# Kernel tuning notes

Hardware: AMD Instinct MI355X
Metric: run time of the kernel (lower is better)

The kernel has to match this reference:

```python
import jax, jax.numpy as jnp
import numpy as np

GRID_SIZE = 4
ORDER = 3
NUM_BASIS = GRID_SIZE + ORDER  # 7
KNOTS = jnp.linspace(-1.0, 1.0, NUM_BASIS + ORDER + 1)  # 11 knots


def _normalise(x):
    # eval-mode with uninitialized running stats: use batch min/max
    min_val = x.min(axis=0)
    max_val = x.max(axis=0)
    width = jnp.maximum(max_val - min_val, 0.01)
    centre = 0.5 * (max_val + min_val)
    scaled = (x - centre) / (0.5 * width)
    return jnp.clip(scaled, -2.0, 2.0)


def _bspline_basis(x):
    # x: (B, I) -> basis: (B, I, NUM_BASIS), de Boor recursion vectorized over i
    xe = x[..., None]  # (B, I, 1)
    idx = jnp.arange(NUM_BASIS)
    left, right = KNOTS[idx], KNOTS[idx + 1]
    basis = ((xe >= left) & (xe < right)).astype(x.dtype)
    last = jnp.where(xe[..., 0] == KNOTS[NUM_BASIS], 1.0, basis[..., -1])
    basis = basis.at[..., -1].set(last)
    for k in range(1, ORDER + 1):
        d1 = KNOTS[idx + k] - KNOTS[idx]
        d2 = KNOTS[idx + k + 1] - KNOTS[idx + 1]
        b_next = jnp.concatenate([basis[..., 1:], jnp.zeros_like(basis[..., :1])], axis=-1)
        t1 = jnp.where(d1 > 0, (xe - KNOTS[idx]) / jnp.where(d1 > 0, d1, 1.0), 0.0) * basis
        t2 = jnp.where(d2 > 0, (KNOTS[idx + k + 1] - xe) / jnp.where(d2 > 0, d2, 1.0), 0.0) * b_next
        basis = t1 + t2
    return basis


def setup_inputs() -> dict:
    key = jax.random.key(0)
    k1, k2, k3 = jax.random.split(key, 3)
    B, I, O = 8192, 256, 256
    x = jax.random.normal(k1, (B, I), dtype=jnp.float32)
    # xavier-uniform base_weight
    bound = float(np.sqrt(6.0 / (I + O)))
    base_weight = jax.random.uniform(k2, (O, I), minval=-bound, maxval=bound, dtype=jnp.float32)
    spline_weight = jnp.ones((O, I), dtype=jnp.float32)
    spline_coeff = 0.001 * jax.random.normal(k3, (O, I, NUM_BASIS), dtype=jnp.float32)
    bias = jnp.zeros((O,), dtype=jnp.float32)
    return {"x": x, "base_weight": base_weight, "spline_weight": spline_weight,
            "spline_coeff": spline_coeff, "bias": bias}


def reference(x, base_weight, spline_weight, spline_coeff, bias):
    x_norm = _normalise(x)                          # (B, I)
    basis = _bspline_basis(x_norm)                  # (B, I, M)
    silu_x = x_norm * jax.nn.sigmoid(x_norm)        # (B, I)
    base_out = silu_x @ base_weight.T               # sum_i silu_i * W_oi -> (B, O)
    coeff_scaled = spline_coeff * spline_weight[..., None]  # (O, I, M)
    spline_out = jnp.einsum('bim,oim->bo', basis, coeff_scaled)
    return base_out + spline_out + bias[None, :]
```

## Files before the change

### kernel.cpp

```cpp
#include <hip/hip_runtime.h>
#include <hip/hip_bf16.h>

#define B_SZ 8192
#define I_SZ 256
#define O_SZ 256
#define KDIM 2048
#define BM 32
#define BN 128
#define BKT 64
#define NT 32
#define NPART 128

typedef __bf16 bf16x8 __attribute__((ext_vector_type(8)));
typedef float f32x4 __attribute__((ext_vector_type(4)));

__global__ __launch_bounds__(256) void minmax_partial(
    const float* __restrict__ x, float* __restrict__ pmin,
    float* __restrict__ pmax) {
  const int cg = threadIdx.x & 63;
  const int rs = threadIdx.x >> 6;
  const int r0 = blockIdx.x * 64;
  const float* p = x + (size_t)(r0 + rs) * I_SZ + cg * 4;
  float4 mn = {1e30f, 1e30f, 1e30f, 1e30f};
  float4 mx = {-1e30f, -1e30f, -1e30f, -1e30f};
#pragma unroll
  for (int k = 0; k < 16; ++k) {
    const float4 v = *reinterpret_cast<const float4*>(p + (size_t)k * 4 * I_SZ);
    mn.x = fminf(mn.x, v.x); mn.y = fminf(mn.y, v.y);
    mn.z = fminf(mn.z, v.z); mn.w = fminf(mn.w, v.w);
    mx.x = fmaxf(mx.x, v.x); mx.y = fmaxf(mx.y, v.y);
    mx.z = fmaxf(mx.z, v.z); mx.w = fmaxf(mx.w, v.w);
  }
  __shared__ float rmn[4][I_SZ], rmx[4][I_SZ];
  *reinterpret_cast<float4*>(&rmn[rs][cg * 4]) = mn;
  *reinterpret_cast<float4*>(&rmx[rs][cg * 4]) = mx;
  __syncthreads();
  if (threadIdx.x < 64) {
    float4 a, b;
    const int c0 = threadIdx.x * 4;
    a.x = fminf(fminf(rmn[0][c0+0], rmn[1][c0+0]), fminf(rmn[2][c0+0], rmn[3][c0+0]));
    a.y = fminf(fminf(rmn[0][c0+1], rmn[1][c0+1]), fminf(rmn[2][c0+1], rmn[3][c0+1]));
    a.z = fminf(fminf(rmn[0][c0+2], rmn[1][c0+2]), fminf(rmn[2][c0+2], rmn[3][c0+2]));
    a.w = fminf(fminf(rmn[0][c0+3], rmn[1][c0+3]), fminf(rmn[2][c0+3], rmn[3][c0+3]));
    b.x = fmaxf(fmaxf(rmx[0][c0+0], rmx[1][c0+0]), fmaxf(rmx[2][c0+0], rmx[3][c0+0]));
    b.y = fmaxf(fmaxf(rmx[0][c0+1], rmx[1][c0+1]), fmaxf(rmx[2][c0+1], rmx[3][c0+1]));
    b.z = fmaxf(fmaxf(rmx[0][c0+2], rmx[1][c0+2]), fmaxf(rmx[2][c0+2], rmx[3][c0+2]));
    b.w = fmaxf(fmaxf(rmx[0][c0+3], rmx[1][c0+3]), fmaxf(rmx[2][c0+3], rmx[3][c0+3]));
    *reinterpret_cast<float4*>(&pmin[blockIdx.x * I_SZ + c0]) = a;
    *reinterpret_cast<float4*>(&pmax[blockIdx.x * I_SZ + c0]) = b;
  }
}

__global__ void pack_W(const float* __restrict__ bw,
                       const float* __restrict__ sw,
                       const float* __restrict__ coeff,
                       __hip_bfloat16* __restrict__ W,
                       const float* __restrict__ pmin,
                       const float* __restrict__ pmax,
                       float* __restrict__ cenrhw) {
  const int idx = blockIdx.x * blockDim.x + threadIdx.x;
  const int i = idx & (I_SZ - 1);
  const int o = idx >> 8;
  const float s = sw[idx];
  union { __hip_bfloat16 h[8]; float4 f4; } u;
#pragma unroll
  for (int m = 0; m < 7; ++m)
    u.h[m] = __float2bfloat16(coeff[(size_t)idx * 7 + m] * s);
  u.h[7] = __float2bfloat16(bw[idx]);
  const size_t off = (size_t)o * KDIM + (size_t)((i ^ (o & 7)) << 3);
  *reinterpret_cast<float4*>(&W[off]) = u.f4;

  if (blockIdx.x == 0) {
    const int c = threadIdx.x;
    float mn = 1e30f, mx = -1e30f;
#pragma unroll 8
    for (int p = 0; p < NPART; ++p) {
      mn = fminf(mn, pmin[p * I_SZ + c]);
      mx = fmaxf(mx, pmax[p * I_SZ + c]);
    }
    const float width = fmaxf(mx - mn, 0.01f);
    const float rhw = 2.0f / width;
    cenrhw[2 * c]     = rhw;
    cenrhw[2 * c + 1] = -0.5f * (mx + mn) * rhw;
  }
}

__device__ __forceinline__ void async16(const __hip_bfloat16* g, __hip_bfloat16* l) {
  __builtin_amdgcn_global_load_lds(
      (const __attribute__((address_space(1))) void*)g,
      (__attribute__((address_space(3))) void*)l, 16, 0, 0);
}

__global__ __launch_bounds__(256, 2) void gemm_fused(
    const float* __restrict__ x, const __hip_bfloat16* __restrict__ W,
    const float* __restrict__ cenrhw, const float* __restrict__ bias,
    float* __restrict__ out) {
  __shared__ __align__(16) __hip_bfloat16 Alds[2][BM * BKT];
  __shared__ __align__(16) __hip_bfloat16 Blds[2][BN * BKT];
  __shared__ float2 scl[I_SZ];

  const int t = threadIdx.x;
  const int lane = t & 63;
  const int wave = t >> 6;
  const int fr = lane & 15, fk = lane >> 4;

  const int bid = blockIdx.x;
  const int swz = (bid & 7) * 64 + (bid >> 3);
  const int bm = swz >> 1, bn = swz & 1;
  const int r0 = bm * BM;
  const int c0 = bn * BN;

  scl[t] = reinterpret_cast<const float2*>(cenrhw)[t];

  const int arow = t >> 3;
  const int af_  = t & 7;
  const float* xp = x + (size_t)(r0 + arow) * I_SZ + af_;

  const __hip_bfloat16* gb0 = W + (size_t)(c0 + (t >> 3)) * KDIM + (t & 7) * 8;

  f32x4 acc[2][2] = {{{0.f,0.f,0.f,0.f},{0.f,0.f,0.f,0.f}},
                     {{0.f,0.f,0.f,0.f},{0.f,0.f,0.f,0.f}}};

  auto stageB = [&](int buf, int kt) {
    const size_t k0 = (size_t)kt * BKT;
    async16(gb0 + k0,                      &Blds[buf][t * 8]);
    async16(gb0 + k0 + (size_t)32 * KDIM,  &Blds[buf][2048 + t * 8]);
    async16(gb0 + k0 + (size_t)64 * KDIM,  &Blds[buf][4096 + t * 8]);
    async16(gb0 + k0 + (size_t)96 * KDIM,  &Blds[buf][6144 + t * 8]);
  };

  auto buildA = [&](int buf, int kt, float xv) {
    const float2 s2 = scl[kt * 8 + af_];
    const float xn = __builtin_fmaf(xv, s2.x, s2.y);
    const float sp = __builtin_fmaf(xn, 5.0f, 5.0f);
    const float cf = floorf(sp);
    const float c6 = fminf(cf, 6.0f);
    const int ci = (int)c6;
    const float u = sp - c6;
    const float zm = (sp > 7.0f) ? 0.0f : (1.0f / 6.0f);
    const float u2 = u * u;
    const float u3 = u2 * u;
    const float t1 = 1.0f - u;
    const float q3 = u3 * zm;
    const float q0 = (t1 * t1) * (t1 * zm);
    float h2 = __builtin_fmaf(-3.0f, u, 3.0f);
    h2 = __builtin_fmaf(h2, u, 3.0f);
    h2 = __builtin_fmaf(h2, u, 1.0f);
    const float q2 = h2 * zm;
    float h1 = __builtin_fmaf(3.0f, u, -6.0f);
    h1 = __builtin_fmaf(h1, u2, 4.0f);
    const float q1 = h1 * zm;
    const float silu = xn * __builtin_amdgcn_rcpf(1.0f + __expf(-xn));
    union { __hip_bfloat16 h[8]; float4 f4; } uu;
#pragma unroll
    for (int j = 0; j < 7; ++j) {
      float v = 0.0f;
      v = (ci == j + 3) ? q0 : v;
      v = (ci == j + 2) ? q1 : v;
      v = (ci == j + 1) ? q2 : v;
      v = (ci == j)     ? q3 : v;
      uu.h[j] = __float2bfloat16(v);
    }
    uu.h[7] = __float2bfloat16(silu);
    const int unit = af_ ^ (arow & 7);
    *reinterpret_cast<float4*>(&Alds[buf][arow * BKT + unit * 8]) = uu.f4;
  };

  auto compute = [&](int buf) {
    bf16x8 af[2][2], bg[2][2];
#pragma unroll
    for (int m = 0; m < 2; ++m)
#pragma unroll
      for (int kk = 0; kk < 2; ++kk) {
        const int row = m * 16 + fr;
        const int unit = ((kk << 2) | fk) ^ (row & 7);
        af[m][kk] = *reinterpret_cast<const bf16x8*>(&Alds[buf][row * BKT + unit * 8]);
      }
#pragma unroll
    for (int n = 0; n < 2; ++n)
#pragma unroll
      for (int kk = 0; kk < 2; ++kk) {
        const int row = wave * 32 + n * 16 + fr;
        const int unit = ((kk << 2) | fk) ^ (row & 7);
        bg[n][kk] = *reinterpret_cast<const bf16x8*>(&Blds[buf][row * BKT + unit * 8]);
      }
#pragma unroll
    for (int kk = 0; kk < 2; ++kk)
#pragma unroll
      for (int m = 0; m < 2; ++m)
#pragma unroll
        for (int n = 0; n < 2; ++n)
          acc[m][n] = __builtin_amdgcn_mfma_f32_16x16x32_bf16(
              af[m][kk], bg[n][kk], acc[m][n], 0, 0, 0);
  };

  const float xv0 = xp[0];
  float xpf = xp[8];
  __syncthreads();
  stageB(0, 0);
  buildA(0, 0, xv0);
  __syncthreads();
  int cur = 0;
  for (int kt = 0; kt < NT - 1; ++kt) {
    stageB(cur ^ 1, kt + 1);
    const float xpf2 = xp[min(kt + 2, NT - 1) * 8];
    buildA(cur ^ 1, kt + 1, xpf);
    compute(cur);
    __syncthreads();
    xpf = xpf2;
    cur ^= 1;
  }
  compute(cur);

#pragma unroll
  for (int m = 0; m < 2; ++m)
#pragma unroll
    for (int n = 0; n < 2; ++n) {
      const int col = c0 + wave * 32 + n * 16 + fr;
      const float bc = bias[col];
#pragma unroll
      for (int r = 0; r < 4; ++r) {
        const int row = r0 + m * 16 + fk * 4 + r;
        out[(size_t)row * O_SZ + col] = acc[m][n][r] + bc;
      }
    }
}

extern "C" void kernel_launch(void* const* d_in, const int* in_sizes, int n_in,
                              void* d_out, int out_size, void* d_ws, size_t ws_size,
                              hipStream_t stream) {
  const float* x     = (const float*)d_in[0];
  const float* bw    = (const float*)d_in[1];
  const float* sw    = (const float*)d_in[2];
  const float* coeff = (const float*)d_in[3];
  const float* bias  = (const float*)d_in[4];
  float* out = (float*)d_out;

  char* ws = (char*)d_ws;
  __hip_bfloat16* Wbuf = (__hip_bfloat16*)ws;
  float* pmin   = (float*)(ws + (size_t)O_SZ * KDIM * 2);
  float* pmax   = pmin + NPART * I_SZ;
  float* cenrhw = pmax + NPART * I_SZ;

  minmax_partial<<<NPART, 256, 0, stream>>>(x, pmin, pmax);
  pack_W<<<(O_SZ * I_SZ) / 256, 256, 0, stream>>>(bw, sw, coeff, Wbuf,
                                                  pmin, pmax, cenrhw);
  gemm_fused<<<(B_SZ / BM) * (O_SZ / BN), 256, 0, stream>>>(x, Wbuf, cenrhw,
                                                            bias, out);
}
```

Before: 42.31 us.

## Build spline/SiLU A operand in registers and widen K tile to 128

```diff
diff --git a/kernel.cpp b/kernel.cpp
--- a/kernel.cpp
+++ b/kernel.cpp
@@ -7,8 +7,8 @@
 #define KDIM 2048
 #define BM 32
 #define BN 128
-#define BKT 64
-#define NT 32
+#define KTO 128
+#define NTO 16
 #define NPART 128
 
 typedef __bf16 bf16x8 __attribute__((ext_vector_type(8)));
@@ -95,8 +95,7 @@
     const float* __restrict__ x, const __hip_bfloat16* __restrict__ W,
     const float* __restrict__ cenrhw, const float* __restrict__ bias,
     float* __restrict__ out) {
-  __shared__ __align__(16) __hip_bfloat16 Alds[2][BM * BKT];
-  __shared__ __align__(16) __hip_bfloat16 Blds[2][BN * BKT];
+  __shared__ __align__(16) __hip_bfloat16 Blds[2][BN * KTO];
   __shared__ float2 scl[I_SZ];
 
   const int t = threadIdx.x;
@@ -112,29 +111,26 @@
 
   scl[t] = reinterpret_cast<const float2*>(cenrhw)[t];
 
-  const int arow = t >> 3;
-  const int af_  = t & 7;
-  const float* xp = x + (size_t)(r0 + arow) * I_SZ + af_;
-
-  const __hip_bfloat16* gb0 = W + (size_t)(c0 + (t >> 3)) * KDIM + (t & 7) * 8;
+  const __hip_bfloat16* gbase =
+      W + (size_t)(c0 + (t >> 4)) * KDIM + (t & 15) * 8;
+
+  auto stageB = [&](int buf, int kt) {
+    const __hip_bfloat16* g = gbase + kt * KTO;
+    __hip_bfloat16* l = &Blds[buf][t * 8];
+#pragma unroll
+    for (int q = 0; q < 8; ++q)
+      async16(g + (size_t)16 * q * KDIM, l + 2048 * q);
+  };
+
+  const float* xq = x + (size_t)(r0 + fr) * I_SZ + fk;
 
   f32x4 acc[2][2] = {{{0.f,0.f,0.f,0.f},{0.f,0.f,0.f,0.f}},
                      {{0.f,0.f,0.f,0.f},{0.f,0.f,0.f,0.f}}};
 
-  auto stageB = [&](int buf, int kt) {
-    const size_t k0 = (size_t)kt * BKT;
-    async16(gb0 + k0,                      &Blds[buf][t * 8]);
-    async16(gb0 + k0 + (size_t)32 * KDIM,  &Blds[buf][2048 + t * 8]);
-    async16(gb0 + k0 + (size_t)64 * KDIM,  &Blds[buf][4096 + t * 8]);
-    async16(gb0 + k0 + (size_t)96 * KDIM,  &Blds[buf][6144 + t * 8]);
-  };
-
-  auto buildA = [&](int buf, int kt, float xv) {
-    const float2 s2 = scl[kt * 8 + af_];
+  auto evalOne = [&](float xv, float2 s2) -> bf16x8 {
     const float xn = __builtin_fmaf(xv, s2.x, s2.y);
     const float sp = __builtin_fmaf(xn, 5.0f, 5.0f);
-    const float cf = floorf(sp);
-    const float c6 = fminf(cf, 6.0f);
+    const float c6 = fminf(floorf(sp), 6.0f);
     const int ci = (int)c6;
     const float u = sp - c6;
     const float zm = (sp > 7.0f) ? 0.0f : (1.0f / 6.0f);
@@ -151,7 +147,7 @@
     h1 = __builtin_fmaf(h1, u2, 4.0f);
     const float q1 = h1 * zm;
     const float silu = xn * __builtin_amdgcn_rcpf(1.0f + __expf(-xn));
-    union { __hip_bfloat16 h[8]; float4 f4; } uu;
+    union { __hip_bfloat16 h[8]; bf16x8 v; } uu;
 #pragma unroll
     for (int j = 0; j < 7; ++j) {
       float v = 0.0f;
@@ -162,55 +158,57 @@
       uu.h[j] = __float2bfloat16(v);
     }
     uu.h[7] = __float2bfloat16(silu);
-    const int unit = af_ ^ (arow & 7);
-    *reinterpret_cast<float4*>(&Alds[buf][arow * BKT + unit * 8]) = uu.f4;
+    return uu.v;
   };
 
-  auto compute = [&](int buf) {
-    bf16x8 af[2][2], bg[2][2];
-#pragma unroll
-    for (int m = 0; m < 2; ++m)
-#pragma unroll
-      for (int kk = 0; kk < 2; ++kk) {
-        const int row = m * 16 + fr;
-        const int unit = ((kk << 2) | fk) ^ (row & 7);
-        af[m][kk] = *reinterpret_cast<const bf16x8*>(&Alds[buf][row * BKT + unit * 8]);
+  auto computeTile = [&](int buf, int kt, const float (&xv)[8]) {
+    const __hip_bfloat16* L = Blds[buf];
+    const int brow = wave * 32 + fr;
+    const int bswz = brow & 7;
+#pragma unroll
+    for (int ss = 0; ss < 4; ++ss) {
+      const float2 s2 = scl[kt * 16 + ss * 4 + fk];
+      const bf16x8 a0 = evalOne(xv[ss], s2);
+      const bf16x8 a1 = evalOne(xv[4 + ss], s2);
+      const int u = ((ss << 2) | fk) ^ bswz;
+      const bf16x8 b0 =
+          *reinterpret_cast<const bf16x8*>(&L[brow * KTO + u * 8]);
+      const bf16x8 b1 =
+          *reinterpret_cast<const bf16x8*>(&L[(brow + 16) * KTO + u * 8]);
+      acc[0][0] = __builtin_amdgcn_mfma_f32_16x16x32_bf16(a0, b0, acc[0][0], 0, 0, 0);
+      acc[0][1] = __builtin_amdgcn_mfma_f32_16x16x32_bf16(a0, b1, acc[0][1], 0, 0, 0);
+      acc[1][0] = __builtin_amdgcn_mfma_f32_16x16x32_bf16(a1, b0, acc[1][0], 0, 0, 0);
+      acc[1][1] = __builtin_amdgcn_mfma_f32_16x16x32_bf16(a1, b1, acc[1][1], 0, 0, 0);
+    }
+  };
+
+  float xva[8], xvb[8];
+#pragma unroll
+  for (int j = 0; j < 4; ++j) {
+    xva[j]     = xq[j * 4];
+    xva[4 + j] = xq[16 * I_SZ + j * 4];
+  }
+  stageB(0, 0);
+  __syncthreads();
+
+  for (int kt = 0; kt < NTO; ++kt) {
+    const int buf = kt & 1;
+    if (kt + 1 < NTO) {
+      stageB(buf ^ 1, kt + 1);
+      const int o = (kt + 1) * 16;
+#pragma unroll
+      for (int j = 0; j < 4; ++j) {
+        xvb[j]     = xq[o + j * 4];
+        xvb[4 + j] = xq[16 * I_SZ + o + j * 4];
       }
-#pragma unroll
-    for (int n = 0; n < 2; ++n)
-#pragma unroll
-      for (int kk = 0; kk < 2; ++kk) {
-        const int row = wave * 32 + n * 16 + fr;
-        const int unit = ((kk << 2) | fk) ^ (row & 7);
-        bg[n][kk] = *reinterpret_cast<const bf16x8*>(&Blds[buf][row * BKT + unit * 8]);
-      }
-#pragma unroll
-    for (int kk = 0; kk < 2; ++kk)
-#pragma unroll
-      for (int m = 0; m < 2; ++m)
-#pragma unroll
-        for (int n = 0; n < 2; ++n)
-          acc[m][n] = __builtin_amdgcn_mfma_f32_16x16x32_bf16(
-              af[m][kk], bg[n][kk], acc[m][n], 0, 0, 0);
-  };
-
-  const float xv0 = xp[0];
-  float xpf = xp[8];
-  __syncthreads();
-  stageB(0, 0);
-  buildA(0, 0, xv0);
-  __syncthreads();
-  int cur = 0;
-  for (int kt = 0; kt < NT - 1; ++kt) {
-    stageB(cur ^ 1, kt + 1);
-    const float xpf2 = xp[min(kt + 2, NT - 1) * 8];
-    buildA(cur ^ 1, kt + 1, xpf);
-    compute(cur);
-    __syncthreads();
-    xpf = xpf2;
-    cur ^= 1;
-  }
-  compute(cur);
+    }
+    computeTile(buf, kt, xva);
+    if (kt + 1 < NTO) {
+      __syncthreads();
+#pragma unroll
+      for (int j = 0; j < 8; ++j) xva[j] = xvb[j];
+    }
+  }
 
 #pragma unroll
   for (int m = 0; m < 2; ++m)
```

Measured after the change: 76.12 us. 1.8x slower.

## Halve GEMM N-tile to 64 and use a 2x2 wave layout

Applied to the files above, without the earlier changes.

```diff
diff --git a/kernel.cpp b/kernel.cpp
--- a/kernel.cpp
+++ b/kernel.cpp
@@ -6,7 +6,7 @@
 #define O_SZ 256
 #define KDIM 2048
 #define BM 32
-#define BN 128
+#define BN 64
 #define BKT 64
 #define NT 32
 #define NPART 128
@@ -91,7 +91,7 @@
       (__attribute__((address_space(3))) void*)l, 16, 0, 0);
 }
 
-__global__ __launch_bounds__(256, 2) void gemm_fused(
+__global__ __launch_bounds__(256, 4) void gemm_fused(
     const float* __restrict__ x, const __hip_bfloat16* __restrict__ W,
     const float* __restrict__ cenrhw, const float* __restrict__ bias,
     float* __restrict__ out) {
@@ -102,13 +102,13 @@
   const int t = threadIdx.x;
   const int lane = t & 63;
   const int wave = t >> 6;
+  const int wm = wave >> 1, wn = wave & 1;
   const int fr = lane & 15, fk = lane >> 4;
 
   const int bid = blockIdx.x;
-  const int swz = (bid & 7) * 64 + (bid >> 3);
-  const int bm = swz >> 1, bn = swz & 1;
-  const int r0 = bm * BM;
-  const int c0 = bn * BN;
+  const int swz = (bid & 7) * 128 + (bid >> 3);
+  const int bm = swz >> 2, bn = swz & 3;
+  const int r0 = bm * BM, c0 = bn * BN;
 
   scl[t] = reinterpret_cast<const float2*>(cenrhw)[t];
 
@@ -118,29 +118,23 @@
 
   const __hip_bfloat16* gb0 = W + (size_t)(c0 + (t >> 3)) * KDIM + (t & 7) * 8;
 
-  f32x4 acc[2][2] = {{{0.f,0.f,0.f,0.f},{0.f,0.f,0.f,0.f}},
-                     {{0.f,0.f,0.f,0.f},{0.f,0.f,0.f,0.f}}};
+  f32x4 acc[2] = {{0.f,0.f,0.f,0.f},{0.f,0.f,0.f,0.f}};
 
   auto stageB = [&](int buf, int kt) {
     const size_t k0 = (size_t)kt * BKT;
-    async16(gb0 + k0,                      &Blds[buf][t * 8]);
-    async16(gb0 + k0 + (size_t)32 * KDIM,  &Blds[buf][2048 + t * 8]);
-    async16(gb0 + k0 + (size_t)64 * KDIM,  &Blds[buf][4096 + t * 8]);
-    async16(gb0 + k0 + (size_t)96 * KDIM,  &Blds[buf][6144 + t * 8]);
+    async16(gb0 + k0,                     &Blds[buf][t * 8]);
+    async16(gb0 + k0 + (size_t)32 * KDIM, &Blds[buf][2048 + t * 8]);
   };
 
   auto buildA = [&](int buf, int kt, float xv) {
     const float2 s2 = scl[kt * 8 + af_];
     const float xn = __builtin_fmaf(xv, s2.x, s2.y);
     const float sp = __builtin_fmaf(xn, 5.0f, 5.0f);
-    const float cf = floorf(sp);
-    const float c6 = fminf(cf, 6.0f);
+    const float c6 = fminf(floorf(sp), 6.0f);
     const int ci = (int)c6;
     const float u = sp - c6;
     const float zm = (sp > 7.0f) ? 0.0f : (1.0f / 6.0f);
-    const float u2 = u * u;
-    const float u3 = u2 * u;
-    const float t1 = 1.0f - u;
+    const float u2 = u * u, u3 = u2 * u, t1 = 1.0f - u;
     const float q3 = u3 * zm;
     const float q0 = (t1 * t1) * (t1 * zm);
     float h2 = __builtin_fmaf(-3.0f, u, 3.0f);
@@ -167,31 +161,27 @@
   };
 
   auto compute = [&](int buf) {
-    bf16x8 af[2][2], bg[2][2];
-#pragma unroll
-    for (int m = 0; m < 2; ++m)
+    bf16x8 af[2], bg[2][2];
+#pragma unroll
+    for (int kk = 0; kk < 2; ++kk) {
+      const int row = wm * 16 + fr;
+      const int unit = ((kk << 2) | fk) ^ (row & 7);
+      af[kk] = *reinterpret_cast<const bf16x8*>(&Alds[buf][row * BKT + unit * 8]);
+    }
+#pragma unroll
+    for (int n = 0; n < 2; ++n)
 #pragma unroll
       for (int kk = 0; kk < 2; ++kk) {
-        const int row = m * 16 + fr;
-        const int unit = ((kk << 2) | fk) ^ (row & 7);
-        af[m][kk] = *reinterpret_cast<const bf16x8*>(&Alds[buf][row * BKT + unit * 8]);
-      }
-#pragma unroll
-    for (int n = 0; n < 2; ++n)
-#pragma unroll
-      for (int kk = 0; kk < 2; ++kk) {
-        const int row = wave * 32 + n * 16 + fr;
+        const int row = wn * 32 + n * 16 + fr;
         const int unit = ((kk << 2) | fk) ^ (row & 7);
         bg[n][kk] = *reinterpret_cast<const bf16x8*>(&Blds[buf][row * BKT + unit * 8]);
       }
 #pragma unroll
     for (int kk = 0; kk < 2; ++kk)
 #pragma unroll
-      for (int m = 0; m < 2; ++m)
-#pragma unroll
-        for (int n = 0; n < 2; ++n)
-          acc[m][n] = __builtin_amdgcn_mfma_f32_16x16x32_bf16(
-              af[m][kk], bg[n][kk], acc[m][n], 0, 0, 0);
+      for (int n = 0; n < 2; ++n)
+        acc[n] = __builtin_amdgcn_mfma_f32_16x16x32_bf16(
+            af[kk], bg[n][kk], acc[n], 0, 0, 0);
   };
 
   const float xv0 = xp[0];
@@ -213,17 +203,15 @@
   compute(cur);
 
 #pragma unroll
-  for (int m = 0; m < 2; ++m)
-#pragma unroll
-    for (int n = 0; n < 2; ++n) {
-      const int col = c0 + wave * 32 + n * 16 + fr;
-      const float bc = bias[col];
-#pragma unroll
-      for (int r = 0; r < 4; ++r) {
-        const int row = r0 + m * 16 + fk * 4 + r;
-        out[(size_t)row * O_SZ + col] = acc[m][n][r] + bc;
-      }
-    }
+  for (int n = 0; n < 2; ++n) {
+    const int col = c0 + wn * 32 + n * 16 + fr;
+    const float bc = bias[col];
+#pragma unroll
+    for (int r = 0; r < 4; ++r) {
+      const int row = r0 + wm * 16 + fk * 4 + r;
+      out[(size_t)row * O_SZ + col] = acc[n][r] + bc;
+    }
+  }
 }
 
 extern "C" void kernel_launch(void* const* d_in, const int* in_sizes, int n_in,
```

After: 44.89 us. 6.1% more time.
